# Optimization experiments

Hardware: AMD Instinct MI355X
Metric: run time of the kernel (lower is better)

The kernel has to match this reference:

```python
import jax, jax.numpy as jnp
import numpy as np


def setup_inputs() -> dict:
    key = jax.random.key(0)
    k1, k2, k3 = jax.random.split(key, 3)
    B, L, I = 128, 512, 1024
    doc_rep = jax.random.normal(k1, (B, L, I), dtype=jnp.float32)
    # torch.nn.Linear(input_size, label_size): weight (L, I), bias (L,)
    W = jax.random.normal(k2, (L, I), dtype=jnp.float32) * (1.0 / np.sqrt(I))
    b = jax.random.normal(k3, (L,), dtype=jnp.float32) * 0.01
    return {"doc_rep": doc_rep, "W": W, "b": b}


def reference(doc_rep, W, b):
    # Original: full Linear -> (B, L, L), then take diagonal over last two dims.
    # Diagonal of (doc_rep @ W.T + b) is exactly the per-label dot product:
    # out[b, l] = doc_rep[b, l, :] . W[l, :] + b[l]
    logits = jnp.einsum('bli,li->bl', doc_rep, W) + b
    return jax.nn.sigmoid(logits)
```

## Files before the change

### kernel.cpp

```cpp
#include <hip/hip_runtime.h>


#define B_DIM 128
#define L_DIM 512
#define I_DIM 1024
#define WPB 8
#define DEPTH 4

typedef float vfloat4 __attribute__((ext_vector_type(4)));

__global__ __launch_bounds__(256, 4) void labelwise_mlc_kernel(
    const float* __restrict__ doc,
    const float* __restrict__ W,
    const float* __restrict__ bias,
    float* __restrict__ out)
{
    const int wave = (blockIdx.x * 256 + threadIdx.x) >> 6;
    const int lane = threadIdx.x & 63;
    const int l  = wave & (L_DIM - 1);
    const int b0 = (wave >> 9) * WPB;

    const vfloat4* __restrict__ wp = (const vfloat4*)(W + (size_t)l * I_DIM);
    vfloat4 w[4];
#pragma unroll
    for (int k = 0; k < 4; ++k) w[k] = wp[lane + 64 * k];
    const float bl = bias[l];

    const float* dbase = doc + ((size_t)b0 * L_DIM + l) * I_DIM;
    const size_t rstride = (size_t)L_DIM * I_DIM;

    vfloat4 buf[DEPTH][4];
#pragma unroll
    for (int j = 0; j < DEPTH; ++j) {
        const vfloat4* dp = (const vfloat4*)(dbase + (size_t)j * rstride);
#pragma unroll
        for (int k = 0; k < 4; ++k)
            buf[j][k] = __builtin_nontemporal_load(dp + lane + 64 * k);
    }

    float acc[WPB];
#pragma unroll
    for (int j = 0; j < WPB; ++j) {
        const int s = j & (DEPTH - 1);
        float a0 = 0.0f, a1 = 0.0f;
#pragma unroll
        for (int k = 0; k < 2; ++k) {
            a0 = fmaf(buf[s][k].x, w[k].x, a0);
            a0 = fmaf(buf[s][k].y, w[k].y, a0);
            a0 = fmaf(buf[s][k].z, w[k].z, a0);
            a0 = fmaf(buf[s][k].w, w[k].w, a0);
        }
#pragma unroll
        for (int k = 2; k < 4; ++k) {
            a1 = fmaf(buf[s][k].x, w[k].x, a1);
            a1 = fmaf(buf[s][k].y, w[k].y, a1);
            a1 = fmaf(buf[s][k].z, w[k].z, a1);
            a1 = fmaf(buf[s][k].w, w[k].w, a1);
        }
        acc[j] = a0 + a1;
        if (j + DEPTH < WPB) {
            const vfloat4* dp =
                (const vfloat4*)(dbase + (size_t)(j + DEPTH) * rstride);
#pragma unroll
            for (int k = 0; k < 4; ++k)
                buf[s][k] = __builtin_nontemporal_load(dp + lane + 64 * k);
        }
    }

    const bool hi5 = (lane & 32) != 0;
    float r[4];
#pragma unroll
    for (int i = 0; i < 4; ++i) {
        const float mine = hi5 ? acc[i + 4] : acc[i];
        const float send = hi5 ? acc[i] : acc[i + 4];
        r[i] = mine + __shfl_xor(send, 32, 64);
    }
    const bool hi4 = (lane & 16) != 0;
    float s2[2];
#pragma unroll
    for (int i = 0; i < 2; ++i) {
        const float mine = hi4 ? r[i + 2] : r[i];
        const float send = hi4 ? r[i] : r[i + 2];
        s2[i] = mine + __shfl_xor(send, 16, 64);
    }
    const bool hi3 = (lane & 8) != 0;
    {
        const float mine = hi3 ? s2[1] : s2[0];
        const float send = hi3 ? s2[0] : s2[1];
        s2[0] = mine + __shfl_xor(send, 8, 64);
    }
    s2[0] += __shfl_xor(s2[0], 4, 64);
    s2[0] += __shfl_xor(s2[0], 2, 64);
    s2[0] += __shfl_xor(s2[0], 1, 64);

    if ((lane & 7) == 0) {
        const int j = lane >> 3;
        const float v = s2[0] + bl;
        out[(size_t)(b0 + j) * L_DIM + l] = 1.0f / (1.0f + __expf(-v));
    }
}

extern "C" void kernel_launch(void* const* d_in, const int* in_sizes, int n_in,
                              void* d_out, int out_size, void* d_ws, size_t ws_size,
                              hipStream_t stream) {
    const float* doc  = (const float*)d_in[0];
    const float* W    = (const float*)d_in[1];
    const float* bias = (const float*)d_in[2];
    float* out = (float*)d_out;

    const int blocks = (L_DIM * (B_DIM / WPB)) / 4;
    labelwise_mlc_kernel<<<blocks, 256, 0, stream>>>(doc, W, bias, out);
}
```

Before: 330.3 us.

## Map each block to a contiguous 8-label slab of one batch row

Each block now handles one batch index and 8 consecutive labels. It reads a contiguous 32KB slab of doc plus the matching W slab, with all 256 threads striding across it, and reduces across waves through shared memory. Previously each wave reused one W row across 8 batch rows that sat far apart in memory, using software pipelining. The new layout gives fully sequential doc reads and a larger grid, but W is now reloaded for every batch row (relying on cache) and a block-level sync is added.

```diff
diff --git a/kernel.cpp b/kernel.cpp
--- a/kernel.cpp
+++ b/kernel.cpp
@@ -4,67 +4,43 @@
 #define B_DIM 128
 #define L_DIM 512
 #define I_DIM 1024
-#define WPB 8
-#define DEPTH 4
+#define LG 8
 
 typedef float vfloat4 __attribute__((ext_vector_type(4)));
 
-__global__ __launch_bounds__(256, 4) void labelwise_mlc_kernel(
+__global__ __launch_bounds__(256) void labelwise_mlc_kernel(
     const float* __restrict__ doc,
     const float* __restrict__ W,
     const float* __restrict__ bias,
     float* __restrict__ out)
 {
-    const int wave = (blockIdx.x * 256 + threadIdx.x) >> 6;
-    const int lane = threadIdx.x & 63;
-    const int l  = wave & (L_DIM - 1);
-    const int b0 = (wave >> 9) * WPB;
+    const int t    = threadIdx.x;
+    const int lane = t & 63;
+    const int wid  = t >> 6;
+    const int lg   = blockIdx.x & (L_DIM / LG - 1);
+    const int b    = blockIdx.x >> 6;
 
-    const vfloat4* __restrict__ wp = (const vfloat4*)(W + (size_t)l * I_DIM);
-    vfloat4 w[4];
+    const vfloat4* __restrict__ dp = (const vfloat4*)doc +
+        (size_t)b * (L_DIM * I_DIM / 4) + (size_t)lg * (LG * I_DIM / 4);
+    const vfloat4* __restrict__ wp = (const vfloat4*)W +
+        (size_t)lg * (LG * I_DIM / 4);
+
+    vfloat4 d[LG], w[LG];
 #pragma unroll
-    for (int k = 0; k < 4; ++k) w[k] = wp[lane + 64 * k];
-    const float bl = bias[l];
-
-    const float* dbase = doc + ((size_t)b0 * L_DIM + l) * I_DIM;
-    const size_t rstride = (size_t)L_DIM * I_DIM;
-
-    vfloat4 buf[DEPTH][4];
-#pragma unroll
-    for (int j = 0; j < DEPTH; ++j) {
-        const vfloat4* dp = (const vfloat4*)(dbase + (size_t)j * rstride);
-#pragma unroll
-        for (int k = 0; k < 4; ++k)
-            buf[j][k] = __builtin_nontemporal_load(dp + lane + 64 * k);
+    for (int k = 0; k < LG; ++k) {
+        const int o = k * 256 + t;
+        d[k] = __builtin_nontemporal_load(dp + o);
+        w[k] = wp[o];
     }
 
-    float acc[WPB];
+    float acc[LG];
 #pragma unroll
-    for (int j = 0; j < WPB; ++j) {
-        const int s = j & (DEPTH - 1);
-        float a0 = 0.0f, a1 = 0.0f;
-#pragma unroll
-        for (int k = 0; k < 2; ++k) {
-            a0 = fmaf(buf[s][k].x, w[k].x, a0);
-            a0 = fmaf(buf[s][k].y, w[k].y, a0);
-            a0 = fmaf(buf[s][k].z, w[k].z, a0);
-            a0 = fmaf(buf[s][k].w, w[k].w, a0);
-        }
-#pragma unroll
-        for (int k = 2; k < 4; ++k) {
-            a1 = fmaf(buf[s][k].x, w[k].x, a1);
-            a1 = fmaf(buf[s][k].y, w[k].y, a1);
-            a1 = fmaf(buf[s][k].z, w[k].z, a1);
-            a1 = fmaf(buf[s][k].w, w[k].w, a1);
-        }
-        acc[j] = a0 + a1;
-        if (j + DEPTH < WPB) {
-            const vfloat4* dp =
-                (const vfloat4*)(dbase + (size_t)(j + DEPTH) * rstride);
-#pragma unroll
-            for (int k = 0; k < 4; ++k)
-                buf[s][k] = __builtin_nontemporal_load(dp + lane + 64 * k);
-        }
+    for (int k = 0; k < LG; ++k) {
+        float a = d[k].x * w[k].x;
+        a = fmaf(d[k].y, w[k].y, a);
+        a = fmaf(d[k].z, w[k].z, a);
+        a = fmaf(d[k].w, w[k].w, a);
+        acc[k] = a;
     }
 
     const bool hi5 = (lane & 32) != 0;
@@ -84,19 +60,31 @@
         s2[i] = mine + __shfl_xor(send, 16, 64);
     }
     const bool hi3 = (lane & 8) != 0;
+    float s0;
     {
         const float mine = hi3 ? s2[1] : s2[0];
         const float send = hi3 ? s2[0] : s2[1];
-        s2[0] = mine + __shfl_xor(send, 8, 64);
+        s0 = mine + __shfl_xor(send, 8, 64);
     }
-    s2[0] += __shfl_xor(s2[0], 4, 64);
-    s2[0] += __shfl_xor(s2[0], 2, 64);
-    s2[0] += __shfl_xor(s2[0], 1, 64);
+    s0 += __shfl_xor(s0, 4, 64);
+    s0 += __shfl_xor(s0, 2, 64);
+    s0 += __shfl_xor(s0, 1, 64);
 
-    if ((lane & 7) == 0) {
-        const int j = lane >> 3;
-        const float v = s2[0] + bl;
-        out[(size_t)(b0 + j) * L_DIM + l] = 1.0f / (1.0f + __expf(-v));
+    __shared__ float part[LG][4];
+    if ((lane & 7) == 0) part[lane >> 3][wid] = s0;
+    __syncthreads();
+
+    if (t < 32) {
+        const int m = t >> 2;
+        const int wv = t & 3;
+        float v = part[m][wv];
+        v += __shfl_xor(v, 1, 64);
+        v += __shfl_xor(v, 2, 64);
+        if (wv == 0) {
+            const int l = lg * LG + m;
+            const float z = v + bias[l];
+            out[(size_t)b * L_DIM + l] = 1.0f / (1.0f + __expf(-z));
+        }
     }
 }
 
@@ -108,6 +96,6 @@
     const float* bias = (const float*)d_in[2];
     float* out = (float*)d_out;
 
-    const int blocks = (L_DIM * (B_DIM / WPB)) / 4;
+    const int blocks = B_DIM * (L_DIM / LG);
     labelwise_mlc_kernel<<<blocks, 256, 0, stream>>>(doc, W, bias, out);
 }
```

Measured after the change: 334.5 us. About the same (+1.2%).
